# Kernel tuning notes

Hardware: AMD Instinct MI355X
Metric: run time of the kernel (lower is better)

## Reference

```python
import jax, jax.numpy as jnp
import numpy as np

D, H, R = 1024, 16, 16
HD = D // H          # head dim 64
I = 2816             # 256*ceil(int(1024*4*2/3)/256)


def _rms(x, eps=1e-6):
    return x * jax.lax.rsqrt(jnp.mean(jnp.square(x), -1, keepdims=True) + eps)


def _act_quant(x):
    # per-token absmax int8 quant (BitNet b1.58 activation quant)
    s = 127.0 / jnp.clip(jnp.max(jnp.abs(x), -1, keepdims=True), 1e-5)
    return jnp.clip(jnp.round(x * s), -128.0, 127.0) / s


def _w_quant(w):
    # ternary {-1,0,1} weight quant with per-tensor absmean scale
    s = 1.0 / jnp.clip(jnp.mean(jnp.abs(w)), 1e-5)
    return jnp.clip(jnp.round(w * s), -1.0, 1.0) / s


def bitlinear(x, w, b=None):
    # StandardBitLinear: RMSNorm -> STE activation quant -> STE ternary weight quant -> linear
    xn = _rms(x)
    xq = xn + jax.lax.stop_gradient(_act_quant(xn) - xn)
    wq = w + jax.lax.stop_gradient(_w_quant(w) - w)
    y = xq @ wq.T
    return y + b if b is not None else y


def layernorm(x, g, b, eps=1e-5):
    m = jnp.mean(x, -1, keepdims=True)
    v = jnp.mean(jnp.square(x - m), -1, keepdims=True)
    return (x - m) * jax.lax.rsqrt(v + eps) * g + b


def modulate(x, shift, scale):
    return x * (1.0 + scale[:, None, :]) + shift[:, None, :]


def dora_attn(q_in, wqkv, mag, la, lb, wp):
    # NOTE: faithful to source — qkv all derive from `query`; key/value args unused.
    B, N, C = q_in.shape
    qkv = bitlinear(q_in, wqkv).reshape(B, N, 3, H, HD).transpose(2, 0, 3, 1, 4)
    q, k, v = qkv[0], qkv[1], qkv[2]                      # [B,H,N,HD]
    delta = (q_in @ la.T) @ lb.T                          # LoRA delta [B,N,C]
    q = q + mag * delta.reshape(B, N, H, HD).transpose(0, 2, 1, 3)
    attn = jax.nn.softmax(jnp.einsum('bhnd,bhmd->bhnm', q, k) * (HD ** -0.5), axis=-1)
    out = jnp.einsum('bhnm,bhmd->bhnd', attn, v).transpose(0, 2, 1, 3).reshape(B, N, C)
    return bitlinear(out, wp)


def hgrn_attn(x, wi, wf, wg, wo, gn):
    # HGRN fused_recurrent: h_t = f_t * h_{t-1} + i_t (elementwise linear recurrence)
    B, N, C = x.shape
    f = jax.nn.sigmoid(bitlinear(x, wf))
    i = jax.nn.silu(bitlinear(x, wi)) * (1.0 - f)

    def step(h, ifp):
        it, ft = ifp
        h = ft * h + it
        return h, h

    _, hs = jax.lax.scan(step, jnp.zeros((B, C), x.dtype),
                         (i.transpose(1, 0, 2), f.transpose(1, 0, 2)))
    o = hs.transpose(1, 0, 2)                             # [B,N,C]
    g = bitlinear(x, wg)
    o = _rms(o) * gn * g * jax.nn.sigmoid(g)              # RMSNormSwishGate
    return bitlinear(o, wo)


def bit_mlp(x, wgate, wdown):
    y = bitlinear(x, wgate)
    gate, y = jnp.split(y, 2, axis=-1)
    return bitlinear(jax.nn.silu(gate) * y, wdown)


def setup_inputs() -> dict:
    key = jax.random.key(0)
    ks = iter(jax.random.split(key, 64))

    def nrm(shape, scale=0.02):
        return jax.random.normal(next(ks), shape, jnp.float32) * scale

    B, N, M = 4, 1024, 256
    inp = {
        'x': jax.random.normal(next(ks), (B, N, D), jnp.float32),
        'y': jax.random.normal(next(ks), (B, M, D), jnp.float32),
        'c': jax.random.normal(next(ks), (B, D), jnp.float32),
        'ada_w': nrm((6 * D, D)), 'ada_b': jnp.zeros((6 * D,), jnp.float32),
        'lnx_g': jnp.ones((D,), jnp.float32), 'lnx_b': jnp.zeros((D,), jnp.float32),
        'lny_g': jnp.ones((D,), jnp.float32), 'lny_b': jnp.zeros((D,), jnp.float32),
        'cax_wqkv': nrm((3 * D, D)), 'cax_mag': jnp.ones((1, H, 1, 1), jnp.float32),
        'cax_la': nrm((R, D)), 'cax_lb': nrm((D, R)), 'cax_wp': nrm((D, D)),
        'cay_wqkv': nrm((3 * D, D)), 'cay_mag': jnp.ones((1, H, 1, 1), jnp.float32),
        'cay_la': nrm((R, D)), 'cay_lb': nrm((D, R)), 'cay_wp': nrm((D, D)),
        'ax_wi': nrm((D, D)), 'ax_wf': nrm((D, D)), 'ax_wg': nrm((D, D)),
        'ax_wo': nrm((D, D)), 'ax_gn': jnp.ones((D,), jnp.float32),
        'ay_wi': nrm((D, D)), 'ay_wf': nrm((D, D)), 'ay_wg': nrm((D, D)),
        'ay_wo': nrm((D, D)), 'ay_gn': jnp.ones((D,), jnp.float32),
        'mx_wg': nrm((2 * I, D)), 'mx_wd': nrm((D, I)),
        'my_wg': nrm((2 * I, D)), 'my_wd': nrm((D, I)),
    }
    return inp


def reference(x, y, c, ada_w, ada_b, lnx_g, lnx_b, lny_g, lny_b,
              cax_wqkv, cax_mag, cax_la, cax_lb, cax_wp,
              cay_wqkv, cay_mag, cay_la, cay_lb, cay_wp,
              ax_wi, ax_wf, ax_wg, ax_wo, ax_gn,
              ay_wi, ay_wf, ay_wg, ay_wo, ay_gn,
              mx_wg, mx_wd, my_wg, my_wd):
    mod = bitlinear(jax.nn.silu(c), ada_w, ada_b)
    shift_msa, scale_msa, gate_msa, shift_mlp, scale_mlp, gate_mlp = jnp.split(mod, 6, axis=1)
    xn = layernorm(x, lnx_g, lnx_b)
    yn = layernorm(y, lny_g, lny_b)
    g1 = gate_msa[:, None, :]
    x = x + g1 * dora_attn(xn, cax_wqkv, cax_mag, cax_la, cax_lb, cax_wp)
    y = y + g1 * dora_attn(yn, cay_wqkv, cay_mag, cay_la, cay_lb, cay_wp)
    x = x + g1 * hgrn_attn(modulate(xn, shift_msa, scale_msa), ax_wi, ax_wf, ax_wg, ax_wo, ax_gn)
    y = y + g1 * hgrn_attn(modulate(yn, shift_msa, scale_msa), ay_wi, ay_wf, ay_wg, ay_wo, ay_gn)
    g2 = gate_mlp[:, None, :]
    x = x + g2 * bit_mlp(modulate(layernorm(x, lnx_g, lnx_b), shift_mlp, scale_mlp), mx_wg, mx_wd)
    y = y + g2 * bit_mlp(modulate(layernorm(y, lny_g, lny_b), shift_mlp, scale_mlp), my_wg, my_wd)
    return (x, y)
```

## Files before the change

kernel.cpp:

```cpp
#include <hip/hip_runtime.h>

typedef unsigned short u16;
typedef unsigned int u32;
typedef __bf16 bf8 __attribute__((ext_vector_type(8)));
typedef float f32x4 __attribute__((ext_vector_type(4)));

#define DD 1024

__device__ __forceinline__ u16 f2bf(float x){
  u32 u = __float_as_uint(x);
  u += 0x7fff + ((u >> 16) & 1);
  return (u16)(u >> 16);
}
__device__ __forceinline__ float wred_sum(float v){
  #pragma unroll
  for(int m=32;m;m>>=1) v += __shfl_xor(v,m);
  return v;
}
__device__ __forceinline__ float wred_max(float v){
  #pragma unroll
  for(int m=32;m;m>>=1) v = fmaxf(v,__shfl_xor(v,m));
  return v;
}
__device__ __forceinline__ double wred_sum_d(double v){
  #pragma unroll
  for(int m=32;m;m>>=1) v += __shfl_xor(v,m);
  return v;
}
__device__ __forceinline__ void gload16(const void* g, void* l){
  __builtin_amdgcn_global_load_lds(
      (const __attribute__((address_space(1))) u32*)g,
      (__attribute__((address_space(3))) u32*)l, 16, 0, 0);
}

struct WT { const float* p[17]; u32 n4[17]; u32 off4[17]; };

__global__ void k_wabs_all(WT wt, double* __restrict__ wsum){
  int j = blockIdx.y;
  const float4* w = (const float4*)wt.p[j];
  u32 n4 = wt.n4[j];
  double s = 0.0;
  for(u32 i=blockIdx.x*256+threadIdx.x; i<n4; i+=gridDim.x*256){
    float4 v = w[i];
    s += (double)(fabsf(v.x)+fabsf(v.y)) + (double)(fabsf(v.z)+fabsf(v.w));
  }
  s = wred_sum_d(s);
  __shared__ double red[4];
  if((threadIdx.x&63)==0) red[threadIdx.x>>6]=s;
  __syncthreads();
  if(threadIdx.x==0) atomicAdd(wsum+j, red[0]+red[1]+red[2]+red[3]);
}

struct Counts{ float c[17]; };
__global__ void k_wfin(const double* __restrict__ wsum, float* __restrict__ wscale,
                       float* __restrict__ wrecip, Counts cnt, int nw){
  int j = threadIdx.x;
  if(j < nw){
    float m = (float)(wsum[j] / (double)cnt.c[j]);
    m = fmaxf(m, 1e-5f);
    wscale[j] = m;
    wrecip[j] = 1.f/m;
  }
}

__global__ void k_wquant_all(WT wt, const float* __restrict__ wrecip, u16* __restrict__ wq){
  int j = blockIdx.y;
  const float4* w = (const float4*)wt.p[j];
  uint2* outq = (uint2*)(wq + 4ull*wt.off4[j]);
  u32 n4 = wt.n4[j];
  float s = wrecip[j];
  for(u32 i=blockIdx.x*256+threadIdx.x; i<n4; i+=gridDim.x*256){
    float4 v = w[i];
    float a0 = fminf(fmaxf(rintf(v.x*s),-1.f),1.f);
    float a1 = fminf(fmaxf(rintf(v.y*s),-1.f),1.f);
    float a2 = fminf(fmaxf(rintf(v.z*s),-1.f),1.f);
    float a3 = fminf(fmaxf(rintf(v.w*s),-1.f),1.f);
    u32 p0 = (u32)f2bf(a0) | ((u32)f2bf(a1)<<16);
    u32 p1 = (u32)f2bf(a2) | ((u32)f2bf(a3)<<16);
    outq[i] = make_uint2(p0,p1);
  }
}

__global__ void k_quant(const float* __restrict__ in, int ld, int K, int rpb,
                        const float* __restrict__ msh, const float* __restrict__ msc,
                        int mode,
                        u16* __restrict__ outq, float* __restrict__ rowsc){
  __shared__ float xr[2816];
  __shared__ float red[8];
  int r = blockIdx.x;
  const float* src = in + (size_t)r*ld;
  int b = r / rpb;
  float ss = 0.f, am = 0.f;
  for(int k=threadIdx.x; k<K; k+=256){
    float x = src[k];
    if(mode==1) x = x / (1.f + __expf(-x));
    else if(mode==2){ float yv = src[k+K]; x = (x/(1.f+__expf(-x)))*yv; }
    if(msh) x = x*(1.f + msc[(size_t)b*6144 + k]) + msh[(size_t)b*6144 + k];
    xr[k] = x;
    ss += x*x; am = fmaxf(am, fabsf(x));
  }
  ss = wred_sum(ss); am = wred_max(am);
  if((threadIdx.x&63)==0){ red[threadIdx.x>>6]=ss; red[4+(threadIdx.x>>6)]=am; }
  __syncthreads();
  ss = red[0]+red[1]+red[2]+red[3];
  am = fmaxf(fmaxf(red[4],red[5]),fmaxf(red[6],red[7]));
  float rinv = 1.f / sqrtf(ss/(float)K + 1e-6f);
  float amn = fmaxf(am*rinv, 1e-5f);
  float s = 127.f/amn;
  if(threadIdx.x==0) rowsc[r] = amn/127.f;
  for(int k=threadIdx.x; k<K; k+=256){
    float xn = xr[k]*rinv;
    float q = rintf(xn*s);
    q = fminf(fmaxf(q,-128.f),127.f);
    outq[(size_t)r*K + k] = f2bf(q);
  }
}

__global__ void k_ln(const float* __restrict__ in, const float* __restrict__ g,
                     const float* __restrict__ bt, float* __restrict__ outp){
  __shared__ float xr[1024];
  __shared__ float red[4];
  int r = blockIdx.x;
  const float* src = in + (size_t)r*1024;
  float s1 = 0.f;
  for(int k=threadIdx.x;k<1024;k+=256){ float x=src[k]; xr[k]=x; s1+=x; }
  s1 = wred_sum(s1);
  if((threadIdx.x&63)==0) red[threadIdx.x>>6]=s1;
  __syncthreads();
  float m = (red[0]+red[1]+red[2]+red[3])*(1.f/1024.f);
  float s2 = 0.f;
  for(int k=threadIdx.x;k<1024;k+=256){ float d=xr[k]-m; s2+=d*d; }
  s2 = wred_sum(s2);
  __syncthreads();
  if((threadIdx.x&63)==0) red[threadIdx.x>>6]=s2;
  __syncthreads();
  float v = (red[0]+red[1]+red[2]+red[3])*(1.f/1024.f);
  float rstd = rsqrtf(v + 1e-5f);
  for(int k=threadIdx.x;k<1024;k+=256)
    outp[(size_t)r*1024+k] = (xr[k]-m)*rstd*g[k] + bt[k];
}

__global__ void k_copy(const float* __restrict__ in, float* __restrict__ out, size_t n4){
  size_t i = (size_t)blockIdx.x*256+threadIdx.x;
  if(i<n4) ((float4*)out)[i] = ((const float4*)in)[i];
}

__global__ __launch_bounds__(256) void k_gemm(
    const u16* __restrict__ Aq, const float* __restrict__ arow,
    const u16* __restrict__ Wq, const float* __restrict__ wsc, int wshift,
    int M, int N, int K, int mode, int ntshift,
    const float* __restrict__ bias, const float* __restrict__ gate,
    const float* __restrict__ t16, const float* __restrict__ lb,
    const float* __restrict__ mag,
    u16* __restrict__ qb, u16* __restrict__ kb, u16* __restrict__ vb,
    float* __restrict__ out){
  __shared__ __align__(16) u16 As[128*64];
  __shared__ __align__(16) u16 Bs[128*64];
  int tid = threadIdx.x;
  int lane = tid & 63;
  int w = tid >> 6;
  int gy = (M+127)>>7;
  int nwg = gridDim.x;
  int q8 = nwg>>3, r8 = nwg&7;
  int xcd = blockIdx.x&7, off8 = blockIdx.x>>3;
  int tile = (xcd<r8 ? xcd*(q8+1) : r8*(q8+1) + (xcd-r8)*q8) + off8;
  int tn = (tile/gy)*128;
  int tm = (tile%gy)*128;
  int wr = (w>>1)*64, wc = (w&1)*64;
  f32x4 acc[4][4];
  #pragma unroll
  for(int i=0;i<4;i++)
    #pragma unroll
    for(int j=0;j<4;j++) acc[i][j] = (f32x4){0.f,0.f,0.f,0.f};
  int lr = lane >> 3;
  int lk = (lane & 7) * 8;
  int nk = K >> 6;
  for(int kt=0; kt<nk; ++kt){
    __syncthreads();
    int k0 = kt*64 + lk;
    #pragma unroll
    for(int i=0;i<4;i++){
      int r = (i*4 + w)*8 + lr;
      int gr = tm + r; gr = gr < M ? gr : M-1;
      gload16(Aq + (size_t)gr*K + k0, (char*)As + (i*4+w)*1024);
      int gc = tn + r;
      gload16(Wq + (size_t)gc*K + k0, (char*)Bs + (i*4+w)*1024);
    }
    asm volatile("s_waitcnt vmcnt(0)" ::: "memory");
    __syncthreads();
    #pragma unroll
    for(int kk=0;kk<2;kk++){
      bf8 af[4], bfr[4];
      int kc = kk*32 + ((lane>>4)<<3);
      #pragma unroll
      for(int i=0;i<4;i++){
        af[i]  = *(const bf8*)&As[(wr + i*16 + (lane&15))*64 + kc];
        bfr[i] = *(const bf8*)&Bs[(wc + i*16 + (lane&15))*64 + kc];
      }
      #pragma unroll
      for(int i=0;i<4;i++)
        #pragma unroll
        for(int j=0;j<4;j++)
          acc[i][j] = __builtin_amdgcn_mfma_f32_16x16x32_bf16(af[i], bfr[j], acc[i][j], 0,0,0);
    }
  }
  int r0 = (lane>>4)*4;
  int cc = lane & 15;
  int Nt = 1 << ntshift;
  #pragma unroll
  for(int i=0;i<4;i++){
    int rb = tm + wr + i*16 + r0;
    #pragma unroll
    for(int j=0;j<4;j++){
      int c = tn + wc + j*16 + cc;
      float wsv = wsc[c>>wshift];
      #pragma unroll
      for(int q=0;q<4;q++){
        int r = rb + q;
        if(r < M){
          float v = acc[i][j][q] * arow[r] * wsv;
          if(mode == 0) out[(size_t)r*N + c] = v;
          else if(mode == 1) out[(size_t)r*N + c] = v + bias[c];
          else if(mode == 2) out[(size_t)r*N + c] += gate[(size_t)(r>>ntshift)*6144 + c] * v;
          else {
            int which = c >> 10, c2 = c & 1023, h = c2 >> 6, d = c2 & 63;
            if(which == 0){
              const float4* tp = (const float4*)(t16 + (size_t)r*16);
              const float4* lp = (const float4*)(lb + (size_t)c2*16);
              float ds = 0.f;
              #pragma unroll
              for(int kk2=0;kk2<4;kk2++){
                float4 a4 = tp[kk2], b4 = lp[kk2];
                ds += a4.x*b4.x + a4.y*b4.y + a4.z*b4.z + a4.w*b4.w;
              }
              v += mag[h]*ds;
            }
            u16* dst = which==0 ? qb : (which==1 ? kb : vb);
            int b = r >> ntshift, n = r & (Nt-1);
            dst[((size_t)(b*16+h)*Nt + n)*64 + d] = f2bf(v);
          }
        }
      }
    }
  }
}

__global__ void k_a1(const float* __restrict__ xn, const float* __restrict__ la,
                     float* __restrict__ t16, int rows){
  int t = blockIdx.x*256 + threadIdx.x;
  int r = t >> 4, n = t & 15;
  if(r >= rows) return;
  const float4* a = (const float4*)(xn + (size_t)r*1024);
  const float4* b = (const float4*)(la + (size_t)n*1024);
  float s = 0.f;
  #pragma unroll 8
  for(int k=0;k<256;k++){
    float4 av=a[k], bv=b[k];
    s += av.x*bv.x + av.y*bv.y + av.z*bv.z + av.w*bv.w;
  }
  t16[(size_t)r*16 + n] = s;
}

__global__ __launch_bounds__(256) void k_attn2(const u16* __restrict__ Qb,
    const u16* __restrict__ Kb, const u16* __restrict__ Vb,
    float* __restrict__ outp, int Nt){
  __shared__ __align__(16) u16 Ks[64*72];
  __shared__ __align__(16) u16 Vt[64*72];
  __shared__ __align__(16) u16 Ps[4*16*72];
  int tid = threadIdx.x, lane = tid&63, w = tid>>6;
  int bh = blockIdx.y;
  int q0 = blockIdx.x*64;
  size_t hb = (size_t)bh*Nt*64;
  bf8 qf[2];
  {
    const u16* qp = Qb + hb + (size_t)(q0 + w*16 + (lane&15))*64 + ((lane>>4)*8);
    qf[0] = *(const bf8*)qp;
    qf[1] = *(const bf8*)(qp+32);
  }
  float m_[4], l_[4];
  f32x4 o_[4];
  #pragma unroll
  for(int r=0;r<4;r++){ m_[r]=-1e30f; l_[r]=0.f; }
  #pragma unroll
  for(int t=0;t<4;t++) o_[t]=(f32x4){0.f,0.f,0.f,0.f};
  int ntiles = Nt >> 6;
  int sn = tid>>2, sc = tid&3;
  for(int kt=0; kt<ntiles; kt++){
    __syncthreads();
    {
      const u16* kg = Kb + hb + (size_t)(kt*64)*64;
      const u16* vg = Vb + hb + (size_t)(kt*64)*64;
      *(uint4*)&Ks[sn*72 + sc*8]      = *(const uint4*)&kg[sn*64 + sc*8];
      *(uint4*)&Ks[sn*72 + sc*8 + 32] = *(const uint4*)&kg[sn*64 + sc*8 + 32];
      uint4 v0 = *(const uint4*)&vg[sn*64 + sc*8];
      uint4 v1 = *(const uint4*)&vg[sn*64 + sc*8 + 32];
      const u16* e0 = (const u16*)&v0; const u16* e1 = (const u16*)&v1;
      #pragma unroll
      for(int j=0;j<8;j++){
        Vt[(sc*8+j)*72 + sn]    = e0[j];
        Vt[(sc*8+32+j)*72 + sn] = e1[j];
      }
    }
    __syncthreads();
    f32x4 s_[4];
    #pragma unroll
    for(int t=0;t<4;t++) s_[t]=(f32x4){0.f,0.f,0.f,0.f};
    #pragma unroll
    for(int c=0;c<2;c++){
      #pragma unroll
      for(int t=0;t<4;t++){
        bf8 kf = *(const bf8*)&Ks[(t*16 + (lane&15))*72 + (lane>>4)*8 + 32*c];
        s_[t] = __builtin_amdgcn_mfma_f32_16x16x32_bf16(qf[c], kf, s_[t], 0,0,0);
      }
    }
    #pragma unroll
    for(int r=0;r<4;r++){
      float mx = fmaxf(fmaxf(s_[0][r], s_[1][r]), fmaxf(s_[2][r], s_[3][r]));
      mx *= 0.125f;
      #pragma unroll
      for(int mk=1; mk<16; mk<<=1) mx = fmaxf(mx, __shfl_xor(mx, mk));
      float mn = fmaxf(m_[r], mx);
      float resc = __expf(m_[r] - mn);
      float ps = 0.f;
      #pragma unroll
      for(int t=0;t<4;t++){
        float p = __expf(s_[t][r]*0.125f - mn);
        Ps[w*1152 + ((lane>>4)*4 + r)*72 + (lane&15) + 16*t] = f2bf(p);
        ps += p;
      }
      #pragma unroll
      for(int mk=1; mk<16; mk<<=1) ps += __shfl_xor(ps, mk);
      l_[r] = l_[r]*resc + ps;
      m_[r] = mn;
      #pragma unroll
      for(int t=0;t<4;t++) o_[t][r] *= resc;
    }
    #pragma unroll
    for(int c=0;c<2;c++){
      bf8 pf = *(const bf8*)&Ps[w*1152 + (lane&15)*72 + (lane>>4)*8 + 32*c];
      #pragma unroll
      for(int dt=0;dt<4;dt++){
        bf8 vf = *(const bf8*)&Vt[(dt*16 + (lane&15))*72 + (lane>>4)*8 + 32*c];
        o_[dt] = __builtin_amdgcn_mfma_f32_16x16x32_bf16(pf, vf, o_[dt], 0,0,0);
      }
    }
  }
  int b = bh >> 4, h = bh & 15;
  #pragma unroll
  for(int r=0;r<4;r++){
    float inv = 1.f/l_[r];
    int qrow = q0 + w*16 + (lane>>4)*4 + r;
    size_t ob = ((size_t)b*Nt + qrow)*1024 + (size_t)h*64;
    #pragma unroll
    for(int dt=0;dt<4;dt++)
      outp[ob + dt*16 + (lane&15)] = o_[dt][r]*inv;
  }
}

__global__ void k_gatei(float* __restrict__ qg, int n){
  int idx = blockIdx.x*256 + threadIdx.x;
  if(idx >= n) return;
  int r = idx >> 10, c = idx & 1023;
  size_t bi = (size_t)r*3072 + c;
  float f = 1.f/(1.f+__expf(-qg[bi+1024]));
  float x = qg[bi];
  float si = x/(1.f+__expf(-x));
  qg[bi] = si*(1.f-f);
  qg[bi+1024] = f;
}
__global__ void k_scan1(const float* __restrict__ iin, const float* __restrict__ fin,
                        int ld, float* __restrict__ Fo, float* __restrict__ Ho, int Nt, int L){
  int c = blockIdx.x*256 + threadIdx.x;
  int ch = blockIdx.y, b = blockIdx.z;
  float h = 0.f, F = 1.f;
  size_t base = ((size_t)b*Nt + (size_t)ch*L)*ld + c;
  for(int t=0;t<L;t++){
    float ft = fin[base + (size_t)t*ld];
    float it = iin[base + (size_t)t*ld];
    h = ft*h + it; F *= ft;
  }
  int CH = Nt/L;
  size_t o = ((size_t)b*CH + ch)*DD + c;
  Fo[o]=F; Ho[o]=h;
}
__global__ void k_scan2(const float* __restrict__ Fo, const float* __restrict__ Ho,
                        float* __restrict__ carry, int CH){
  int id = blockIdx.x*256 + threadIdx.x;
  int b = id>>10, c = id&1023;
  float h = 0.f;
  for(int ch=0; ch<CH; ch++){
    size_t o = ((size_t)b*CH + ch)*DD + c;
    carry[o] = h;
    h = Fo[o]*h + Ho[o];
  }
}
__global__ void k_scan3(const float* __restrict__ iin, const float* __restrict__ fin,
                        int ld, const float* __restrict__ carry, float* __restrict__ oo,
                        int Nt, int L){
  int c = blockIdx.x*256 + threadIdx.x;
  int ch = blockIdx.y, b = blockIdx.z;
  int CH = Nt/L;
  float h = carry[((size_t)b*CH + ch)*DD + c];
  size_t base = ((size_t)b*Nt + (size_t)ch*L)*ld + c;
  size_t obase = ((size_t)b*Nt + (size_t)ch*L)*DD + c;
  for(int t=0;t<L;t++){
    float ft = fin[base + (size_t)t*ld];
    float it = iin[base + (size_t)t*ld];
    h = ft*h + it;
    oo[obase + (size_t)t*DD] = h;
  }
}
__global__ void k_oprime(const float* __restrict__ o, const float* __restrict__ g, int gld,
                         const float* __restrict__ gn, float* __restrict__ outp){
  __shared__ float red[4];
  int r = blockIdx.x;
  float ss = 0.f;
  for(int k=threadIdx.x;k<1024;k+=256){ float v=o[(size_t)r*1024+k]; ss += v*v; }
  ss = wred_sum(ss);
  if((threadIdx.x&63)==0) red[threadIdx.x>>6]=ss;
  __syncthreads();
  float tot = red[0]+red[1]+red[2]+red[3];
  float rinv = 1.f/sqrtf(tot*(1.f/1024.f) + 1e-6f);
  for(int k=threadIdx.x;k<1024;k+=256){
    float gv = g[(size_t)r*gld+k];
    float sig = 1.f/(1.f+__expf(-gv));
    outp[(size_t)r*1024+k] = o[(size_t)r*1024+k]*rinv*gn[k]*gv*sig;
  }
}

extern "C" void kernel_launch(void* const* d_in, const int* in_sizes, int n_in,
                              void* d_out, int out_size, void* d_ws, size_t ws_size,
                              hipStream_t stream){
  const float* X     = (const float*)d_in[0];
  const float* Y     = (const float*)d_in[1];
  const float* C     = (const float*)d_in[2];
  const float* ADA_W = (const float*)d_in[3];
  const float* ADA_B = (const float*)d_in[4];
  const float* LNX_G = (const float*)d_in[5];
  const float* LNX_B = (const float*)d_in[6];
  const float* LNY_G = (const float*)d_in[7];
  const float* LNY_B = (const float*)d_in[8];
  const float* CAX_WQKV=(const float*)d_in[9];
  const float* CAX_MAG =(const float*)d_in[10];
  const float* CAX_LA  =(const float*)d_in[11];
  const float* CAX_LB  =(const float*)d_in[12];
  const float* CAX_WP  =(const float*)d_in[13];
  const float* CAY_WQKV=(const float*)d_in[14];
  const float* CAY_MAG =(const float*)d_in[15];
  const float* CAY_LA  =(const float*)d_in[16];
  const float* CAY_LB  =(const float*)d_in[17];
  const float* CAY_WP  =(const float*)d_in[18];
  const float* AX_WI = (const float*)d_in[19];
  const float* AX_WF = (const float*)d_in[20];
  const float* AX_WG = (const float*)d_in[21];
  const float* AX_WO = (const float*)d_in[22];
  const float* AX_GN = (const float*)d_in[23];
  const float* AY_WI = (const float*)d_in[24];
  const float* AY_WF = (const float*)d_in[25];
  const float* AY_WG = (const float*)d_in[26];
  const float* AY_WO = (const float*)d_in[27];
  const float* AY_GN = (const float*)d_in[28];
  const float* MX_WG = (const float*)d_in[29];
  const float* MX_WD = (const float*)d_in[30];
  const float* MY_WG = (const float*)d_in[31];
  const float* MY_WD = (const float*)d_in[32];

  float* OUTX = (float*)d_out;
  float* OUTY = OUTX + (size_t)4096*1024;

  char* base = (char*)d_ws;
  size_t cur = 0;
  auto alloc = [&](size_t bytes)->char*{
    char* p = base + cur; cur += (bytes + 255) & ~(size_t)255; return p; };
  double* WSUM  = (double*)alloc(32*sizeof(double));
  float* WSCALE = (float*)alloc(32*sizeof(float));
  float* WRECIP = (float*)alloc(32*sizeof(float));
  float* MOD    = (float*)alloc((size_t)4*6144*4);
  float* AROW   = (float*)alloc((size_t)4096*4);
  u16*   WQ     = (u16*)alloc((size_t)40370176*2);
  u16*   AQ     = (u16*)alloc((size_t)4096*2816*2);
  float* XN     = (float*)alloc((size_t)4096*1024*4);
  float* YN     = (float*)alloc((size_t)1024*1024*4);
  float* BUFA   = (float*)alloc((size_t)4096*5632*4);
  float* BUFE   = (float*)alloc((size_t)4096*1024*4);
  float* BUFF   = (float*)alloc((size_t)4096*1024*4);
  float* T16    = (float*)alloc((size_t)4096*16*4);
  float* SCF    = (float*)alloc((size_t)4*16*1024*4);
  float* SCH    = (float*)alloc((size_t)4*16*1024*4);
  float* SCC    = (float*)alloc((size_t)4*16*1024*4);
  (void)ws_size; (void)in_sizes; (void)n_in; (void)out_size;

  u16* Qb = (u16*)BUFA;
  u16* Kb = Qb + (size_t)4194304;
  u16* Vb = Kb + (size_t)4194304;
  float* QG = BUFA;

  const float* wptr[17] = {ADA_W, CAX_WQKV, CAX_WP, CAY_WQKV, CAY_WP,
                           AX_WI, AX_WF, AX_WG, AX_WO,
                           AY_WI, AY_WF, AY_WG, AY_WO,
                           MX_WG, MX_WD, MY_WG, MY_WD};
  const size_t wn[17] = {6291456,3145728,1048576,3145728,1048576,
                         1048576,1048576,1048576,1048576,
                         1048576,1048576,1048576,1048576,
                         5767168,2883584,5767168,2883584};
  size_t woff[17]; { size_t o=0; for(int j=0;j<17;j++){ woff[j]=o; o+=wn[j]; } }

  WT wt; Counts cnt;
  for(int j=0;j<17;j++){
    wt.p[j] = wptr[j]; wt.n4[j] = (u32)(wn[j]/4); wt.off4[j] = (u32)(woff[j]/4);
    cnt.c[j] = (float)wn[j];
  }
  hipMemsetAsync(WSUM, 0, 17*sizeof(double), stream);
  k_wabs_all<<<dim3(64,17),256,0,stream>>>(wt, WSUM);
  k_wfin<<<1,32,0,stream>>>(WSUM, WSCALE, WRECIP, cnt, 17);
  k_wquant_all<<<dim3(128,17),256,0,stream>>>(wt, WRECIP, WQ);

  auto gemm = [&](int slot, const u16* aq, int M, int N, int K, int mode,
                  int wshift, int ntshift,
                  const float* bias, const float* gate,
                  const float* t16, const float* lbm, const float* mag,
                  float* out){
    int nwg = (N/128) * ((M+127)/128);
    k_gemm<<<nwg,256,0,stream>>>(aq, AROW, WQ+woff[slot], WSCALE+slot, wshift,
        M, N, K, mode, ntshift, bias, gate, t16, lbm, mag, Qb, Kb, Vb, out);
  };

  k_quant<<<4,256,0,stream>>>(C, 1024, 1024, 1, nullptr, nullptr, 1, AQ, AROW);
  gemm(0, AQ, 4, 6144, 1024, 1, 13, 10, ADA_B, nullptr, nullptr, nullptr, nullptr, MOD);

  k_ln<<<4096,256,0,stream>>>(X, LNX_G, LNX_B, XN);
  k_ln<<<1024,256,0,stream>>>(Y, LNY_G, LNY_B, YN);
  k_copy<<<4096,256,0,stream>>>(X, OUTX, (size_t)1048576);
  k_copy<<<1024,256,0,stream>>>(Y, OUTY, (size_t)262144);

  const float* G1 = MOD + 2048;
  const float* G2 = MOD + 5120;

  k_quant<<<4096,256,0,stream>>>(XN, 1024, 1024, 1024, nullptr, nullptr, 0, AQ, AROW);
  k_a1<<<256,256,0,stream>>>(XN, CAX_LA, T16, 4096);
  gemm(1, AQ, 4096, 3072, 1024, 3, 13, 10, nullptr, nullptr, T16, CAX_LB, CAX_MAG, nullptr);
  k_attn2<<<dim3(16,64),256,0,stream>>>(Qb, Kb, Vb, BUFF, 1024);
  k_quant<<<4096,256,0,stream>>>(BUFF, 1024, 1024, 1024, nullptr, nullptr, 0, AQ, AROW);
  gemm(2, AQ, 4096, 1024, 1024, 2, 13, 10, nullptr, G1, nullptr, nullptr, nullptr, OUTX);

  k_quant<<<1024,256,0,stream>>>(YN, 1024, 1024, 256, nullptr, nullptr, 0, AQ, AROW);
  k_a1<<<64,256,0,stream>>>(YN, CAY_LA, T16, 1024);
  gemm(3, AQ, 1024, 3072, 1024, 3, 13, 8, nullptr, nullptr, T16, CAY_LB, CAY_MAG, nullptr);
  k_attn2<<<dim3(4,64),256,0,stream>>>(Qb, Kb, Vb, BUFF, 256);
  k_quant<<<1024,256,0,stream>>>(BUFF, 1024, 1024, 256, nullptr, nullptr, 0, AQ, AROW);
  gemm(4, AQ, 1024, 1024, 1024, 2, 13, 8, nullptr, G1, nullptr, nullptr, nullptr, OUTY);

  k_quant<<<4096,256,0,stream>>>(XN, 1024, 1024, 1024, MOD, MOD+1024, 0, AQ, AROW);
  gemm(5, AQ, 4096, 3072, 1024, 0, 10, 10, nullptr, nullptr, nullptr, nullptr, nullptr, QG);
  k_gatei<<<16384,256,0,stream>>>(QG, 4194304);
  k_scan1<<<dim3(4,16,4),256,0,stream>>>(QG, QG+1024, 3072, SCF, SCH, 1024, 64);
  k_scan2<<<16,256,0,stream>>>(SCF, SCH, SCC, 16);
  k_scan3<<<dim3(4,16,4),256,0,stream>>>(QG, QG+1024, 3072, SCC, BUFE, 1024, 64);
  k_oprime<<<4096,256,0,stream>>>(BUFE, QG+2048, 3072, AX_GN, BUFF);
  k_quant<<<4096,256,0,stream>>>(BUFF, 1024, 1024, 1024, nullptr, nullptr, 0, AQ, AROW);
  gemm(8, AQ, 4096, 1024, 1024, 2, 13, 10, nullptr, G1, nullptr, nullptr, nullptr, OUTX);

  k_quant<<<1024,256,0,stream>>>(YN, 1024, 1024, 256, MOD, MOD+1024, 0, AQ, AROW);
  gemm(9, AQ, 1024, 3072, 1024, 0, 10, 8, nullptr, nullptr, nullptr, nullptr, nullptr, QG);
  k_gatei<<<4096,256,0,stream>>>(QG, 1048576);
  k_scan1<<<dim3(4,16,4),256,0,stream>>>(QG, QG+1024, 3072, SCF, SCH, 256, 16);
  k_scan2<<<16,256,0,stream>>>(SCF, SCH, SCC, 16);
  k_scan3<<<dim3(4,16,4),256,0,stream>>>(QG, QG+1024, 3072, SCC, BUFE, 256, 16);
  k_oprime<<<1024,256,0,stream>>>(BUFE, QG+2048, 3072, AY_GN, BUFF);
  k_quant<<<1024,256,0,stream>>>(BUFF, 1024, 1024, 256, nullptr, nullptr, 0, AQ, AROW);
  gemm(12, AQ, 1024, 1024, 1024, 2, 13, 8, nullptr, G1, nullptr, nullptr, nullptr, OUTY);

  k_ln<<<4096,256,0,stream>>>(OUTX, LNX_G, LNX_B, XN);
  k_quant<<<4096,256,0,stream>>>(XN, 1024, 1024, 1024, MOD+3072, MOD+4096, 0, AQ, AROW);
  gemm(13, AQ, 4096, 5632, 1024, 0, 13, 10, nullptr, nullptr, nullptr, nullptr, nullptr, BUFA);
  k_quant<<<4096,256,0,stream>>>(BUFA, 5632, 2816, 1024, nullptr, nullptr, 2, AQ, AROW);
  gemm(14, AQ, 4096, 1024, 2816, 2, 13, 10, nullptr, G2, nullptr, nullptr, nullptr, OUTX);

  k_ln<<<1024,256,0,stream>>>(OUTY, LNY_G, LNY_B, YN);
  k_quant<<<1024,256,0,stream>>>(YN, 1024, 1024, 256, MOD+3072, MOD+4096, 0, AQ, AROW);
  gemm(15, AQ, 1024, 5632, 1024, 0, 13, 8, nullptr, nullptr, nullptr, nullptr, nullptr, BUFA);
  k_quant<<<1024,256,0,stream>>>(BUFA, 5632, 2816, 256, nullptr, nullptr, 2, AQ, AROW);
  gemm(16, AQ, 1024, 1024, 2816, 2, 13, 8, nullptr, G2, nullptr, nullptr, nullptr, OUTY);
}
```

Before: 1.662 ms.

## Double-buffer GEMM LDS tiles with XOR swizzle and split LoRA add into separate kernel

The GEMM now keeps two LDS buffers, issuing the global-to-LDS loads for the next K tile before computing on the current one, and waits with a partial vmcnt so load latency overlaps with MFMA work. The K-column offset inside each LDS row is XOR-swizzled by row to reduce bank conflicts on the fragment reads. The per-element LoRA delta dot product is moved out of the QKV GEMM epilogue into a new elementwise kernel that adds it to the bf16 Q buffer. This adds a launch, an extra read-modify-write of Q, and an extra bf16 rounding step, and doubles the LDS footprint, which can lower occupancy.

```diff
diff --git a/kernel.cpp b/kernel.cpp
--- a/kernel.cpp
+++ b/kernel.cpp
@@ -11,6 +11,10 @@
   u32 u = __float_as_uint(x);
   u += 0x7fff + ((u >> 16) & 1);
   return (u16)(u >> 16);
+}
+__device__ __forceinline__ float bf2f(u16 x){
+  u32 u = ((u32)x) << 16;
+  return __uint_as_float(u);
 }
 __device__ __forceinline__ float wred_sum(float v){
   #pragma unroll
@@ -150,12 +154,10 @@
     const u16* __restrict__ Wq, const float* __restrict__ wsc, int wshift,
     int M, int N, int K, int mode, int ntshift,
     const float* __restrict__ bias, const float* __restrict__ gate,
-    const float* __restrict__ t16, const float* __restrict__ lb,
-    const float* __restrict__ mag,
     u16* __restrict__ qb, u16* __restrict__ kb, u16* __restrict__ vb,
     float* __restrict__ out){
-  __shared__ __align__(16) u16 As[128*64];
-  __shared__ __align__(16) u16 Bs[128*64];
+  __shared__ __align__(16) u16 As[2][128*64];
+  __shared__ __align__(16) u16 Bs[2][128*64];
   int tid = threadIdx.x;
   int lane = tid & 63;
   int w = tid >> 6;
@@ -173,29 +175,29 @@
     #pragma unroll
     for(int j=0;j<4;j++) acc[i][j] = (f32x4){0.f,0.f,0.f,0.f};
   int lr = lane >> 3;
-  int lk = (lane & 7) * 8;
+  int lk = ((lane & 7) ^ lr) * 8;
   int nk = K >> 6;
-  for(int kt=0; kt<nk; ++kt){
-    __syncthreads();
-    int k0 = kt*64 + lk;
+
+  auto stage = [&](int ktile, int buf){
+    int k0 = ktile*64 + lk;
     #pragma unroll
     for(int i=0;i<4;i++){
       int r = (i*4 + w)*8 + lr;
       int gr = tm + r; gr = gr < M ? gr : M-1;
-      gload16(Aq + (size_t)gr*K + k0, (char*)As + (i*4+w)*1024);
+      gload16(Aq + (size_t)gr*K + k0, (char*)&As[buf][0] + (i*4+w)*1024);
       int gc = tn + r;
-      gload16(Wq + (size_t)gc*K + k0, (char*)Bs + (i*4+w)*1024);
+      gload16(Wq + (size_t)gc*K + k0, (char*)&Bs[buf][0] + (i*4+w)*1024);
     }
-    asm volatile("s_waitcnt vmcnt(0)" ::: "memory");
-    __syncthreads();
+  };
+  auto compute = [&](int buf){
     #pragma unroll
     for(int kk=0;kk<2;kk++){
+      int phys = ((kk*4 + (lane>>4)) ^ (lane&7)) * 8;
       bf8 af[4], bfr[4];
-      int kc = kk*32 + ((lane>>4)<<3);
       #pragma unroll
       for(int i=0;i<4;i++){
-        af[i]  = *(const bf8*)&As[(wr + i*16 + (lane&15))*64 + kc];
-        bfr[i] = *(const bf8*)&Bs[(wc + i*16 + (lane&15))*64 + kc];
+        af[i]  = *(const bf8*)&As[buf][(wr + i*16 + (lane&15))*64 + phys];
+        bfr[i] = *(const bf8*)&Bs[buf][(wc + i*16 + (lane&15))*64 + phys];
       }
       #pragma unroll
       for(int i=0;i<4;i++)
@@ -203,7 +205,21 @@
         for(int j=0;j<4;j++)
           acc[i][j] = __builtin_amdgcn_mfma_f32_16x16x32_bf16(af[i], bfr[j], acc[i][j], 0,0,0);
     }
-  }
+  };
+
+  stage(0, 0);
+  int kt = 0;
+  for(; kt < nk-1; ++kt){
+    stage(kt+1, (kt&1)^1);
+    asm volatile("s_waitcnt vmcnt(8)" ::: "memory");
+    __builtin_amdgcn_s_barrier();
+    compute(kt&1);
+    __builtin_amdgcn_s_barrier();
+  }
+  asm volatile("s_waitcnt vmcnt(0)" ::: "memory");
+  __builtin_amdgcn_s_barrier();
+  compute(kt&1);
+
   int r0 = (lane>>4)*4;
   int cc = lane & 15;
   int Nt = 1 << ntshift;
@@ -224,17 +240,6 @@
           else if(mode == 2) out[(size_t)r*N + c] += gate[(size_t)(r>>ntshift)*6144 + c] * v;
           else {
             int which = c >> 10, c2 = c & 1023, h = c2 >> 6, d = c2 & 63;
-            if(which == 0){
-              const float4* tp = (const float4*)(t16 + (size_t)r*16);
-              const float4* lp = (const float4*)(lb + (size_t)c2*16);
-              float ds = 0.f;
-              #pragma unroll
-              for(int kk2=0;kk2<4;kk2++){
-                float4 a4 = tp[kk2], b4 = lp[kk2];
-                ds += a4.x*b4.x + a4.y*b4.y + a4.z*b4.z + a4.w*b4.w;
-              }
-              v += mag[h]*ds;
-            }
             u16* dst = which==0 ? qb : (which==1 ? kb : vb);
             int b = r >> ntshift, n = r & (Nt-1);
             dst[((size_t)(b*16+h)*Nt + n)*64 + d] = f2bf(v);
@@ -259,6 +264,23 @@
     s += av.x*bv.x + av.y*bv.y + av.z*bv.z + av.w*bv.w;
   }
   t16[(size_t)r*16 + n] = s;
+}
+
+__global__ void k_qadd2(u16* __restrict__ qb, const float* __restrict__ t16,
+                        const float* __restrict__ lb, const float* __restrict__ mag,
+                        int ntshift){
+  int c = blockIdx.x*256 + threadIdx.x;
+  int r = blockIdx.y;
+  const float4* a = (const float4*)(t16 + (size_t)r*16);
+  const float4* b = (const float4*)(lb + (size_t)c*16);
+  float s = 0.f;
+  #pragma unroll
+  for(int k=0;k<4;k++){ float4 av=a[k], bv=b[k]; s += av.x*bv.x+av.y*bv.y+av.z*bv.z+av.w*bv.w; }
+  int h = c>>6, d = c&63;
+  int Nt = 1<<ntshift;
+  int bb = r >> ntshift, n = r & (Nt-1);
+  size_t qi = ((size_t)(bb*16+h)*Nt + n)*64 + d;
+  qb[qi] = f2bf(bf2f(qb[qi]) + mag[h]*s);
 }
 
 __global__ __launch_bounds__(256) void k_attn2(const u16* __restrict__ Qb,
@@ -517,16 +539,14 @@
 
   auto gemm = [&](int slot, const u16* aq, int M, int N, int K, int mode,
                   int wshift, int ntshift,
-                  const float* bias, const float* gate,
-                  const float* t16, const float* lbm, const float* mag,
-                  float* out){
+                  const float* bias, const float* gate, float* out){
     int nwg = (N/128) * ((M+127)/128);
     k_gemm<<<nwg,256,0,stream>>>(aq, AROW, WQ+woff[slot], WSCALE+slot, wshift,
-        M, N, K, mode, ntshift, bias, gate, t16, lbm, mag, Qb, Kb, Vb, out);
+        M, N, K, mode, ntshift, bias, gate, Qb, Kb, Vb, out);
   };
 
   k_quant<<<4,256,0,stream>>>(C, 1024, 1024, 1, nullptr, nullptr, 1, AQ, AROW);
-  gemm(0, AQ, 4, 6144, 1024, 1, 13, 10, ADA_B, nullptr, nullptr, nullptr, nullptr, MOD);
+  gemm(0, AQ, 4, 6144, 1024, 1, 13, 10, ADA_B, nullptr, MOD);
 
   k_ln<<<4096,256,0,stream>>>(X, LNX_G, LNX_B, XN);
   k_ln<<<1024,256,0,stream>>>(Y, LNY_G, LNY_B, YN);
@@ -538,47 +558,49 @@
 
   k_quant<<<4096,256,0,stream>>>(XN, 1024, 1024, 1024, nullptr, nullptr, 0, AQ, AROW);
   k_a1<<<256,256,0,stream>>>(XN, CAX_LA, T16, 4096);
-  gemm(1, AQ, 4096, 3072, 1024, 3, 13, 10, nullptr, nullptr, T16, CAX_LB, CAX_MAG, nullptr);
+  gemm(1, AQ, 4096, 3072, 1024, 3, 13, 10, nullptr, nullptr, nullptr);
+  k_qadd2<<<dim3(4,4096),256,0,stream>>>(Qb, T16, CAX_LB, CAX_MAG, 10);
   k_attn2<<<dim3(16,64),256,0,stream>>>(Qb, Kb, Vb, BUFF, 1024);
   k_quant<<<4096,256,0,stream>>>(BUFF, 1024, 1024, 1024, nullptr, nullptr, 0, AQ, AROW);
-  gemm(2, AQ, 4096, 1024, 1024, 2, 13, 10, nullptr, G1, nullptr, nullptr, nullptr, OUTX);
+  gemm(2, AQ, 4096, 1024, 1024, 2, 13, 10, nullptr, G1, OUTX);
 
   k_quant<<<1024,256,0,stream>>>(YN, 1024, 1024, 256, nullptr, nullptr, 0, AQ, AROW);
   k_a1<<<64,256,0,stream>>>(YN, CAY_LA, T16, 1024);
-  gemm(3, AQ, 1024, 3072, 1024, 3, 13, 8, nullptr, nullptr, T16, CAY_LB, CAY_MAG, nullptr);
+  gemm(3, AQ, 1024, 3072, 1024, 3, 13, 8, nullptr, nullptr, nullptr);
+  k_qadd2<<<dim3(4,1024),256,0,stream>>>(Qb, T16, CAY_LB, CAY_MAG, 8);
   k_attn2<<<dim3(4,64),256,0,stream>>>(Qb, Kb, Vb, BUFF, 256);
   k_quant<<<1024,256,0,stream>>>(BUFF, 1024, 1024, 256, nullptr, nullptr, 0, AQ, AROW);
-  gemm(4, AQ, 1024, 1024, 1024, 2, 13, 8, nullptr, G1, nullptr, nullptr, nullptr, OUTY);
+  gemm(4, AQ, 1024, 1024, 1024, 2, 13, 8, nullptr, G1, OUTY);
 
   k_quant<<<4096,256,0,stream>>>(XN, 1024, 1024, 1024, MOD, MOD+1024, 0, AQ, AROW);
-  gemm(5, AQ, 4096, 3072, 1024, 0, 10, 10, nullptr, nullptr, nullptr, nullptr, nullptr, QG);
+  gemm(5, AQ, 4096, 3072, 1024, 0, 10, 10, nullptr, nullptr, QG);
   k_gatei<<<16384,256,0,stream>>>(QG, 4194304);
   k_scan1<<<dim3(4,16,4),256,0,stream>>>(QG, QG+1024, 3072, SCF, SCH, 1024, 64);
   k_scan2<<<16,256,0,stream>>>(SCF, SCH, SCC, 16);
   k_scan3<<<dim3(4,16,4),256,0,stream>>>(QG, QG+1024, 3072, SCC, BUFE, 1024, 64);
   k_oprime<<<4096,256,0,stream>>>(BUFE, QG+2048, 3072, AX_GN, BUFF);
   k_quant<<<4096,256,0,stream>>>(BUFF, 1024, 1024, 1024, nullptr, nullptr, 0, AQ, AROW);
-  gemm(8, AQ, 4096, 1024, 1024, 2, 13, 10, nullptr, G1, nullptr, nullptr, nullptr, OUTX);
+  gemm(8, AQ, 4096, 1024, 1024, 2, 13, 10, nullptr, G1, OUTX);
 
   k_quant<<<1024,256,0,stream>>>(YN, 1024, 1024, 256, MOD, MOD+1024, 0, AQ, AROW);
-  gemm(9, AQ, 1024, 3072, 1024, 0, 10, 8, nullptr, nullptr, nullptr, nullptr, nullptr, QG);
+  gemm(9, AQ, 1024, 3072, 1024, 0, 10, 8, nullptr, nullptr, QG);
   k_gatei<<<4096,256,0,stream>>>(QG, 1048576);
   k_scan1<<<dim3(4,16,4),256,0,stream>>>(QG, QG+1024, 3072, SCF, SCH, 256, 16);
   k_scan2<<<16,256,0,stream>>>(SCF, SCH, SCC, 16);
   k_scan3<<<dim3(4,16,4),256,0,stream>>>(QG, QG+1024, 3072, SCC, BUFE, 256, 16);
   k_oprime<<<1024,256,0,stream>>>(BUFE, QG+2048, 3072, AY_GN, BUFF);
   k_quant<<<1024,256,0,stream>>>(BUFF, 1024, 1024, 256, nullptr, nullptr, 0, AQ, AROW);
-  gemm(12, AQ, 1024, 1024, 1024, 2, 13, 8, nullptr, G1, nullptr, nullptr, nullptr, OUTY);
+  gemm(12, AQ, 1024, 1024, 1024, 2, 13, 8, nullptr, G1, OUTY);
 
   k_ln<<<4096,256,0,stream>>>(OUTX, LNX_G, LNX_B, XN);
   k_quant<<<4096,256,0,stream>>>(XN, 1024, 1024, 1024, MOD+3072, MOD+4096, 0, AQ, AROW);
-  gemm(13, AQ, 4096, 5632, 1024, 0, 13, 10, nullptr, nullptr, nullptr, nullptr, nullptr, BUFA);
+  gemm(13, AQ, 4096, 5632, 1024, 0, 13, 10, nullptr, nullptr, BUFA);
   k_quant<<<4096,256,0,stream>>>(BUFA, 5632, 2816, 1024, nullptr, nullptr, 2, AQ, AROW);
-  gemm(14, AQ, 4096, 1024, 2816, 2, 13, 10, nullptr, G2, nullptr, nullptr, nullptr, OUTX);
+  gemm(14, AQ, 4096, 1024, 2816, 2, 13, 10, nullptr, G2, OUTX);
 
   k_ln<<<1024,256,0,stream>>>(OUTY, LNY_G, LNY_B, YN);
   k_quant<<<1024,256,0,stream>>>(YN, 1024, 1024, 256, MOD+3072, MOD+4096, 0, AQ, AROW);
-  gemm(15, AQ, 1024, 5632, 1024, 0, 13, 8, nullptr, nullptr, nullptr, nullptr, nullptr, BUFA);
+  gemm(15, AQ, 1024, 5632, 1024, 0, 13, 8, nullptr, nullptr, BUFA);
   k_quant<<<1024,256,0,stream>>>(BUFA, 5632, 2816, 256, nullptr, nullptr, 2, AQ, AROW);
-  gemm(16, AQ, 1024, 1024, 2816, 2, 13, 8, nullptr, G2, nullptr, nullptr, nullptr, OUTY);
-}
+  gemm(16, AQ, 1024, 1024, 2816, 2, 13, 8, nullptr, G2, OUTY);
+}
```

Result: faster. 1.526 ms (-8.2%).
